# Kernel tuning notes

Hardware: AMD Instinct MI355X
Metric: run time of the kernel (lower is better)

The kernel has to match this reference:

```python
import jax, jax.numpy as jnp
import numpy as np

NUM_LAYERS = 16
ALPHA = 1.0
EPS = 1e-20

def setup_inputs() -> dict:
    key = jax.random.key(0)
    k1, k2, k3, k4 = jax.random.split(key, 4)
    B, S, M, G = 8, 9, 8, 512
    M2 = M * M
    return {
        "dict_real": jax.random.normal(k1, (B, S, M2, G), dtype=jnp.float32),
        "dict_imag": jax.random.normal(k2, (B, S, M2, G), dtype=jnp.float32),
        "cov_real": jax.random.normal(k3, (B, S, M, M), dtype=jnp.float32),
        "cov_imag": jax.random.normal(k4, (B, S, M, M), dtype=jnp.float32),
    }

def reference(dict_real, dict_imag, cov_real, cov_imag):
    D = (dict_real + 1j * dict_imag).astype(jnp.complex64)   # (B,S,M2,G) dictionary_band
    C = (cov_real + 1j * cov_imag).astype(jnp.complex64)     # (B,S,M,M) covariance matrix
    B, S, M, _ = C.shape
    G = D.shape[-1]
    # covariance_vector = cov.transpose(2,3).reshape(B,S,M2,1)
    r = jnp.swapaxes(C, 2, 3).reshape(B, S, M * M, 1)
    Dh = jnp.conj(jnp.swapaxes(D, 2, 3))                     # (B,S,G,M2)
    DhD = jnp.matmul(Dh, D)                                  # (B,S,G,G) Hermitian PSD
    Dhr = jnp.matmul(Dh, r)                                  # (B,S,G,1)
    # initial spectrum: real part, L2-normalized over grid dim
    res = jnp.real(Dhr).astype(jnp.float32)
    res = res / (jnp.linalg.norm(res, axis=2, keepdims=True) + EPS)
    # gamma = 1 / max|eig(D^H D)|; Hermitian PSD so eigvalsh gives same max magnitude
    eig = jnp.linalg.eigvalsh(DhD)                           # (B,S,G) real
    gamma = 1.0 / jnp.max(jnp.abs(eig), axis=2, keepdims=True)        # (B,S,1)
    lam = 0.5 * jnp.max(jnp.abs(Dhr), axis=2, keepdims=True).reshape(B, S, 1)
    theta = (ALPHA * lam * gamma).reshape(B, S, 1, 1)
    g = gamma.reshape(B, S, 1, 1).astype(jnp.complex64)
    I = jnp.eye(G, dtype=jnp.complex64)
    Wt = I - g * DhD                                         # (B,S,G,G)
    Wer = g * Dhr                                            # We @ r, constant per layer

    def step(res_c, _):
        s = jnp.matmul(Wt, res_c.astype(jnp.complex64)) + Wer
        res_new = jax.nn.relu(jnp.abs(s) - theta)            # soft-shrinkage on magnitude
        return res_new, res_new

    res_final, res_all = jax.lax.scan(step, res, None, length=NUM_LAYERS)
    result_init_all = jnp.moveaxis(res_all, 0, 2)            # (B,S,L,G,1)

    def minmax_norm(x):
        lo = jnp.min(x, axis=2, keepdims=True)
        hi = jnp.max(x, axis=2, keepdims=True)
        return (x - lo) / (hi - lo + EPS)

    result_ave = minmax_norm(jnp.mean(res_final, axis=1, keepdims=True).astype(jnp.float32))
    result = minmax_norm(res_final)
    return (result, result_ave, result_init_all)
```

## Files before the change

kernel.cpp:

```cpp
#include <hip/hip_runtime.h>
#include <math.h>

#define N_SQ   7
#define INV_P  (1.0f / 256.0f)
#define EPS_F  1e-20f
#define PH     72
#define PQ     67
#define PJ     1040

typedef _Float16 h2   __attribute__((ext_vector_type(2)));
typedef _Float16 f16x4 __attribute__((ext_vector_type(4)));
typedef _Float16 f16x8 __attribute__((ext_vector_type(8)));
typedef float    f32x4 __attribute__((ext_vector_type(4)));

__device__ inline float cdot2(h2 a, h2 b, float c) {
#if __has_builtin(__builtin_amdgcn_fdot2)
    return __builtin_amdgcn_fdot2(a, b, c, false);
#else
    return c + (float)a.x * (float)b.x + (float)a.y * (float)b.y;
#endif
}


__global__ __launch_bounds__(512, 1) void ista_main_kernel(
    const float* __restrict__ Dre, const float* __restrict__ Dim,
    const float* __restrict__ Cre, const float* __restrict__ Cim,
    float* __restrict__ out, float* __restrict__ ws)
{
    const int bs = blockIdx.x;
    const int t  = threadIdx.x;
    const int wv = t >> 6;
    const int ln = t & 63;
    const int c16 = ln & 15;
    const int qd  = ln >> 4;
    const float* __restrict__ dre = Dre + (size_t)bs * 32768;
    const float* __restrict__ dim = Dim + (size_t)bs * 32768;

    __shared__ __align__(16) float uBuf[9216];
    _Float16* ShRe = (_Float16*)uBuf;
    _Float16* ShIm = (_Float16*)uBuf + 64 * PH;
    float*    Q1   = uBuf + 4608;
    float*    sP   = uBuf;
    __shared__ __align__(16) float s_res[512];
    __shared__ __align__(16) float s_r[128];
    __shared__ float s_red[16];
    __shared__ float s_scal[8];

    if (t < 64) {
        int i = t >> 3, j = t & 7;
        s_r[2 * t]     = Cre[bs * 64 + j * 8 + i];
        s_r[2 * t + 1] = Cim[bs * 64 + j * 8 + i];
    }
    __syncthreads();

    float dhr_re = 0.f, dhr_im = 0.f;
    #pragma unroll 8
    for (int m = 0; m < 64; ++m) {
        float ar = dre[m * 512 + t], ai = dim[m * 512 + t];
        float rr = s_r[2 * m], ri = s_r[2 * m + 1];
        dhr_re += ar * rr + ai * ri;
        dhr_im += ar * ri - ai * rr;
    }
    {
        float sv = dhr_re * dhr_re;
        float mv = sqrtf(dhr_re * dhr_re + dhr_im * dhr_im);
        for (int off = 32; off; off >>= 1) {
            sv += __shfl_down(sv, off, 64);
            mv = fmaxf(mv, __shfl_down(mv, off, 64));
        }
        if (ln == 0) { s_red[wv] = sv; s_red[8 + wv] = mv; }
        __syncthreads();
        if (t == 0) {
            float ss = 0.f, mm = 0.f;
            for (int k = 0; k < 8; ++k) { ss += s_red[k]; mm = fmaxf(mm, s_red[8 + k]); }
            s_scal[7] = ss; s_scal[2] = mm;
        }
        __syncthreads();
    }
    float res_g = dhr_re / (sqrtf(s_scal[7]) + EPS_F);
    s_res[t] = res_g;

    const int tau0 = 2 * wv, tau1 = 2 * wv + 1;
    const int I0 = tau0 >> 2, J0 = tau0 & 3;
    const int I1 = tau1 >> 2, J1 = tau1 & 3;

    auto epilogue = [&](f32x4 P0, f32x4 Qa0, f32x4 P1, f32x4 Qa1, bool first, bool last) {
        #pragma unroll
        for (int r = 0; r < 4; ++r) {
            Q1[(I0 * 16 + qd * 4 + r) * PQ + J0 * 16 + c16] = Qa0[r];
            Q1[(I1 * 16 + qd * 4 + r) * PQ + J1 * 16 + c16] = Qa1[r];
        }
        float dv = 0.f;
        if (I0 == J0) {
            #pragma unroll
            for (int r = 0; r < 4; ++r) if (qd * 4 + r == c16) dv = fmaxf(dv, fabsf(P0[r]));
        }
        if (I1 == J1) {
            #pragma unroll
            for (int r = 0; r < 4; ++r) if (qd * 4 + r == c16) dv = fmaxf(dv, fabsf(P1[r]));
        }
        for (int off = 32; off; off >>= 1) dv = fmaxf(dv, __shfl_down(dv, off, 64));
        if (ln == 0) s_red[wv] = dv;
        __syncthreads();
        if (t == 0) {
            float m = 0.f;
            for (int k = 0; k < 8; ++k) m = fmaxf(m, s_red[k]);
            s_scal[3] = first ? logf(m) : 2.f * s_scal[3] + logf(m);
            s_scal[4] = 1.f / m;
        }
        __syncthreads();
        float ic = s_scal[4];
        float ci0[4], ci1[4];
        #pragma unroll
        for (int r = 0; r < 4; ++r) {
            ci0[r] = Qa0[r] - Q1[(J0 * 16 + c16) * PQ + I0 * 16 + qd * 4 + r];
            ci1[r] = Qa1[r] - Q1[(J1 * 16 + c16) * PQ + I1 * 16 + qd * 4 + r];
        }
        if (!last) {
            #pragma unroll
            for (int r = 0; r < 4; ++r) {
                ShRe[(I0 * 16 + qd * 4 + r) * PH + J0 * 16 + c16] = (_Float16)(P0[r] * ic);
                ShIm[(I0 * 16 + qd * 4 + r) * PH + J0 * 16 + c16] = (_Float16)(ci0[r] * ic);
                ShRe[(I1 * 16 + qd * 4 + r) * PH + J1 * 16 + c16] = (_Float16)(P1[r] * ic);
                ShIm[(I1 * 16 + qd * 4 + r) * PH + J1 * 16 + c16] = (_Float16)(ci1[r] * ic);
            }
            __syncthreads();
        } else {
            float fr = 0.f;
            #pragma unroll
            for (int r = 0; r < 4; ++r)
                fr += P0[r] * P0[r] + ci0[r] * ci0[r] + P1[r] * P1[r] + ci1[r] * ci1[r];
            fr *= ic * ic;
            for (int off = 32; off; off >>= 1) fr += __shfl_down(fr, off, 64);
            if (ln == 0) s_red[wv] = fr;
            __syncthreads();
            if (t == 0) {
                float fsum = 0.f;
                for (int k = 0; k < 8; ++k) fsum += s_red[k];
                float loglam = (2.f * s_scal[3] + logf(fsum)) * INV_P;
                float gamma = expf(-loglam);
                s_scal[0] = gamma;
                s_scal[1] = 0.5f * s_scal[2] * gamma;
            }
            __syncthreads();
        }
    };

    f32x4 gP0 = {0.f, 0.f, 0.f, 0.f}, gQ0 = {0.f, 0.f, 0.f, 0.f};
    f32x4 gP1 = {0.f, 0.f, 0.f, 0.f}, gQ1 = {0.f, 0.f, 0.f, 0.f};
    {
        const int srow = t >> 4;
        const int scb  = (t & 15) * 4;
        float4 pr0, pi0, pr1, pi1;
        pr0 = *(const float4*)&dre[srow * 512 + scb];
        pi0 = *(const float4*)&dim[srow * 512 + scb];
        pr1 = *(const float4*)&dre[(srow + 32) * 512 + scb];
        pi1 = *(const float4*)&dim[(srow + 32) * 512 + scb];
        for (int ch = 0; ch < 8; ++ch) {
            *(f16x4*)&ShRe[srow * PH + scb] =
                f16x4{(_Float16)pr0.x, (_Float16)pr0.y, (_Float16)pr0.z, (_Float16)pr0.w};
            *(f16x4*)&ShIm[srow * PH + scb] =
                f16x4{(_Float16)pi0.x, (_Float16)pi0.y, (_Float16)pi0.z, (_Float16)pi0.w};
            *(f16x4*)&ShRe[(srow + 32) * PH + scb] =
                f16x4{(_Float16)pr1.x, (_Float16)pr1.y, (_Float16)pr1.z, (_Float16)pr1.w};
            *(f16x4*)&ShIm[(srow + 32) * PH + scb] =
                f16x4{(_Float16)pi1.x, (_Float16)pi1.y, (_Float16)pi1.z, (_Float16)pi1.w};
            if (ch < 7) {
                int gc = (ch + 1) * 64;
                pr0 = *(const float4*)&dre[srow * 512 + gc + scb];
                pi0 = *(const float4*)&dim[srow * 512 + gc + scb];
                pr1 = *(const float4*)&dre[(srow + 32) * 512 + gc + scb];
                pi1 = *(const float4*)&dim[(srow + 32) * 512 + gc + scb];
            }
            __syncthreads();
            #pragma unroll
            for (int ks = 0; ks < 64; ks += 32) {
                f16x8 arI0 = *(const f16x8*)&ShRe[(I0 * 16 + c16) * PH + ks + qd * 8];
                f16x8 aiI0 = *(const f16x8*)&ShIm[(I0 * 16 + c16) * PH + ks + qd * 8];
                f16x8 arJ0 = *(const f16x8*)&ShRe[(J0 * 16 + c16) * PH + ks + qd * 8];
                f16x8 aiJ0 = *(const f16x8*)&ShIm[(J0 * 16 + c16) * PH + ks + qd * 8];
                gP0 = __builtin_amdgcn_mfma_f32_16x16x32_f16(arI0, arJ0, gP0, 0, 0, 0);
                gP0 = __builtin_amdgcn_mfma_f32_16x16x32_f16(aiI0, aiJ0, gP0, 0, 0, 0);
                gQ0 = __builtin_amdgcn_mfma_f32_16x16x32_f16(aiI0, arJ0, gQ0, 0, 0, 0);
                f16x8 arI1 = *(const f16x8*)&ShRe[(I1 * 16 + c16) * PH + ks + qd * 8];
                f16x8 aiI1 = *(const f16x8*)&ShIm[(I1 * 16 + c16) * PH + ks + qd * 8];
                f16x8 arJ1 = *(const f16x8*)&ShRe[(J1 * 16 + c16) * PH + ks + qd * 8];
                f16x8 aiJ1 = *(const f16x8*)&ShIm[(J1 * 16 + c16) * PH + ks + qd * 8];
                gP1 = __builtin_amdgcn_mfma_f32_16x16x32_f16(arI1, arJ1, gP1, 0, 0, 0);
                gP1 = __builtin_amdgcn_mfma_f32_16x16x32_f16(aiI1, aiJ1, gP1, 0, 0, 0);
                gQ1 = __builtin_amdgcn_mfma_f32_16x16x32_f16(aiI1, arJ1, gQ1, 0, 0, 0);
            }
            __syncthreads();
        }
    }
    epilogue(gP0, gQ0, gP1, gQ1, true, false);

    for (int sq = 0; sq < N_SQ; ++sq) {
        f32x4 P0 = {0.f, 0.f, 0.f, 0.f}, Qa0 = {0.f, 0.f, 0.f, 0.f};
        f32x4 P1 = {0.f, 0.f, 0.f, 0.f}, Qa1 = {0.f, 0.f, 0.f, 0.f};
        #pragma unroll
        for (int ks = 0; ks < 64; ks += 32) {
            f16x8 arI0 = *(const f16x8*)&ShRe[(I0 * 16 + c16) * PH + ks + qd * 8];
            f16x8 aiI0 = *(const f16x8*)&ShIm[(I0 * 16 + c16) * PH + ks + qd * 8];
            f16x8 arJ0 = *(const f16x8*)&ShRe[(J0 * 16 + c16) * PH + ks + qd * 8];
            f16x8 aiJ0 = *(const f16x8*)&ShIm[(J0 * 16 + c16) * PH + ks + qd * 8];
            P0  = __builtin_amdgcn_mfma_f32_16x16x32_f16(arI0, arJ0, P0, 0, 0, 0);
            P0  = __builtin_amdgcn_mfma_f32_16x16x32_f16(aiI0, aiJ0, P0, 0, 0, 0);
            Qa0 = __builtin_amdgcn_mfma_f32_16x16x32_f16(aiI0, arJ0, Qa0, 0, 0, 0);
            f16x8 arI1 = *(const f16x8*)&ShRe[(I1 * 16 + c16) * PH + ks + qd * 8];
            f16x8 aiI1 = *(const f16x8*)&ShIm[(I1 * 16 + c16) * PH + ks + qd * 8];
            f16x8 arJ1 = *(const f16x8*)&ShRe[(J1 * 16 + c16) * PH + ks + qd * 8];
            f16x8 aiJ1 = *(const f16x8*)&ShIm[(J1 * 16 + c16) * PH + ks + qd * 8];
            P1  = __builtin_amdgcn_mfma_f32_16x16x32_f16(arI1, arJ1, P1, 0, 0, 0);
            P1  = __builtin_amdgcn_mfma_f32_16x16x32_f16(aiI1, aiJ1, P1, 0, 0, 0);
            Qa1 = __builtin_amdgcn_mfma_f32_16x16x32_f16(aiI1, arJ1, Qa1, 0, 0, 0);
        }
        epilogue(P0, Qa0, P1, Qa1, false, sq == N_SQ - 1);
    }

    h2 dP[8][8];
    #pragma unroll
    for (int k = 0; k < 8; ++k) {
        const float4* pr = (const float4*)&dre[(8 * wv + k) * 512 + 8 * ln];
        const float4* pi = (const float4*)&dim[(8 * wv + k) * 512 + 8 * ln];
        float4 x0 = pr[0], x1 = pr[1], y0 = pi[0], y1 = pi[1];
        dP[k][0] = h2{(_Float16)x0.x, (_Float16)y0.x};
        dP[k][1] = h2{(_Float16)x0.y, (_Float16)y0.y};
        dP[k][2] = h2{(_Float16)x0.z, (_Float16)y0.z};
        dP[k][3] = h2{(_Float16)x0.w, (_Float16)y0.w};
        dP[k][4] = h2{(_Float16)x1.x, (_Float16)y1.x};
        dP[k][5] = h2{(_Float16)x1.y, (_Float16)y1.y};
        dP[k][6] = h2{(_Float16)x1.z, (_Float16)y1.z};
        dP[k][7] = h2{(_Float16)x1.w, (_Float16)y1.w};
    }

    const float gamma = s_scal[0];
    const float theta = s_scal[1];
    float* out_init = out + 40960 + (size_t)bs * 8192;
    const bool b5 = (ln & 32) != 0, b4 = (ln & 16) != 0, b3 = (ln & 8) != 0;

    for (int l = 0; l < 16; ++l) {
        float4 q0 = *(const float4*)&s_res[8 * ln];
        float4 q1 = *(const float4*)&s_res[8 * ln + 4];
        float rsv[8] = {q0.x, q0.y, q0.z, q0.w, q1.x, q1.y, q1.z, q1.w};
        float uR[8] = {0.f}, uI[8] = {0.f};
        #pragma unroll
        for (int j = 0; j < 8; ++j) {
            _Float16 rh = (_Float16)rsv[j];
            h2 hA = h2{rh, (_Float16)0.f};
            h2 hB = h2{(_Float16)0.f, rh};
            #pragma unroll
            for (int k = 0; k < 8; ++k) {
                uR[k] = cdot2(dP[k][j], hA, uR[k]);
                uI[k] = cdot2(dP[k][j], hB, uI[k]);
            }
        }
        float sR4[4], sI4[4];
        #pragma unroll
        for (int k = 0; k < 4; ++k) {
            float sendR = b5 ? uR[k] : uR[k + 4];
            float sendI = b5 ? uI[k] : uI[k + 4];
            float keepR = b5 ? uR[k + 4] : uR[k];
            float keepI = b5 ? uI[k + 4] : uI[k];
            sR4[k] = keepR + __shfl_xor(sendR, 32, 64);
            sI4[k] = keepI + __shfl_xor(sendI, 32, 64);
        }
        float tR2[2], tI2[2];
        #pragma unroll
        for (int k = 0; k < 2; ++k) {
            float sendR = b4 ? sR4[k] : sR4[k + 2];
            float sendI = b4 ? sI4[k] : sI4[k + 2];
            float keepR = b4 ? sR4[k + 2] : sR4[k];
            float keepI = b4 ? sI4[k + 2] : sI4[k];
            tR2[k] = keepR + __shfl_xor(sendR, 16, 64);
            tI2[k] = keepI + __shfl_xor(sendI, 16, 64);
        }
        float fR = (b3 ? tR2[1] : tR2[0]) + __shfl_xor(b3 ? tR2[0] : tR2[1], 8, 64);
        float fI = (b3 ? tI2[1] : tI2[0]) + __shfl_xor(b3 ? tI2[0] : tI2[1], 8, 64);
        fR += __shfl_xor(fR, 4, 64); fI += __shfl_xor(fI, 4, 64);
        fR += __shfl_xor(fR, 2, 64); fI += __shfl_xor(fI, 2, 64);
        fR += __shfl_xor(fR, 1, 64); fI += __shfl_xor(fI, 1, 64);
        h2 hu1[8], hu2[8];
        #pragma unroll
        for (int m = 0; m < 8; ++m) {
            float br = __shfl(fR, 8 * m, 64);
            float bi = __shfl(fI, 8 * m, 64);
            hu1[m] = h2{(_Float16)br, (_Float16)bi};
            hu2[m] = h2{(_Float16)bi, (_Float16)(-br)};
        }
        #pragma unroll
        for (int j = 0; j < 8; ++j) {
            float wr = 0.f, wi = 0.f;
            #pragma unroll
            for (int k = 0; k < 8; ++k) {
                wr = cdot2(dP[k][j], hu1[k], wr);
                wi = cdot2(dP[k][j], hu2[k], wi);
            }
            *(float2*)&sP[j * PJ + wv * 130 + 2 * ln] = make_float2(wr, wi);
        }
        __syncthreads();
        float wR = 0.f, wI = 0.f;
        {
            const float* pp = &sP[(t & 7) * PJ + 2 * (t >> 3)];
            #pragma unroll
            for (int w8 = 0; w8 < 8; ++w8) {
                float2 c = *(const float2*)(pp + w8 * 130);
                wR += c.x; wI += c.y;
            }
        }
        float sre = res_g + gamma * (dhr_re - wR);
        float sim = gamma * (dhr_im - wI);
        float mag = sqrtf(sre * sre + sim * sim);
        res_g = fmaxf(mag - theta, 0.f);
        out_init[l * 512 + t] = res_g;
        s_res[t] = res_g;
        __syncthreads();
    }

    {
        float mn = res_g, mx = res_g;
        for (int off = 32; off; off >>= 1) {
            mn = fminf(mn, __shfl_down(mn, off, 64));
            mx = fmaxf(mx, __shfl_down(mx, off, 64));
        }
        if (ln == 0) { s_red[wv] = mn; s_red[8 + wv] = mx; }
        __syncthreads();
        if (t == 0) {
            float a = s_red[0], b2 = s_red[8];
            for (int k = 1; k < 8; ++k) { a = fminf(a, s_red[k]); b2 = fmaxf(b2, s_red[8 + k]); }
            s_scal[5] = a; s_scal[6] = b2;
        }
        __syncthreads();
        out[bs * 512 + t] = (res_g - s_scal[5]) / (s_scal[6] - s_scal[5] + EPS_F);
        ws[bs * 512 + t] = res_g;
    }
}

__global__ __launch_bounds__(512) void ista_ave_kernel(
    const float* __restrict__ ws, float* __restrict__ out)
{
    const int b = blockIdx.x;
    const int g = threadIdx.x;
    __shared__ float s_red[16];
    __shared__ float s_scal[2];
    float acc = 0.f;
    #pragma unroll
    for (int s = 0; s < 9; ++s) acc += ws[(b * 9 + s) * 512 + g];
    acc *= (1.f / 9.f);
    float mn = acc, mx = acc;
    for (int off = 32; off; off >>= 1) {
        mn = fminf(mn, __shfl_down(mn, off, 64));
        mx = fmaxf(mx, __shfl_down(mx, off, 64));
    }
    if ((g & 63) == 0) { s_red[g >> 6] = mn; s_red[8 + (g >> 6)] = mx; }
    __syncthreads();
    if (g == 0) {
        float a = s_red[0], b2 = s_red[8];
        for (int k = 1; k < 8; ++k) { a = fminf(a, s_red[k]); b2 = fmaxf(b2, s_red[8 + k]); }
        s_scal[0] = a; s_scal[1] = b2;
    }
    __syncthreads();
    out[36864 + b * 512 + g] = (acc - s_scal[0]) / (s_scal[1] - s_scal[0] + EPS_F);
}

extern "C" void kernel_launch(void* const* d_in, const int* in_sizes, int n_in,
                              void* d_out, int out_size, void* d_ws, size_t ws_size,
                              hipStream_t stream) {
    const float* Dre = (const float*)d_in[0];
    const float* Dim = (const float*)d_in[1];
    const float* Cre = (const float*)d_in[2];
    const float* Cim = (const float*)d_in[3];
    float* out = (float*)d_out;
    float* ws  = (float*)d_ws;

    ista_main_kernel<<<72, 512, 0, stream>>>(Dre, Dim, Cre, Cim, out, ws);
    ista_ave_kernel<<<8, 512, 0, stream>>>(ws, out);
}
```

Measured before the change: 134.2 us.

## Restructure ISTA matvec with register-resident dictionary slices and LDS reductions

The per-layer product D^H(D r) is reorganised. Each thread now keeps its grid column of D as packed fp16 pairs in registers, and each wave keeps a 64-grid chunk of D captured from the staged shared-memory tiles. The D·r partials are reduced across waves through LDS by wave 0, then every thread computes its own output with fdot2. This replaces the old shuffle-based butterfly reduction, the global reloads of D, and the cross-wave LDS transpose. It costs about 128 more VGPRs of resident dictionary data and adds a serialised wave-0 reduction step between two barriers.

```diff
diff --git a/kernel.cpp b/kernel.cpp
--- a/kernel.cpp
+++ b/kernel.cpp
@@ -6,10 +6,8 @@
 #define EPS_F  1e-20f
 #define PH     72
 #define PQ     67
-#define PJ     1040
-
-typedef _Float16 h2   __attribute__((ext_vector_type(2)));
-typedef _Float16 f16x4 __attribute__((ext_vector_type(4)));
+
+typedef _Float16 h2    __attribute__((ext_vector_type(2)));
 typedef _Float16 f16x8 __attribute__((ext_vector_type(8)));
 typedef float    f32x4 __attribute__((ext_vector_type(4)));
 
@@ -20,6 +18,9 @@
     return c + (float)a.x * (float)b.x + (float)a.y * (float)b.y;
 #endif
 }
+__device__ inline h2 bch2(unsigned int x) { return __builtin_bit_cast(h2, x); }
+__device__ inline h2 bch2f(float x)       { return __builtin_bit_cast(h2, x); }
+__device__ inline float bcf(h2 x)         { return __builtin_bit_cast(float, x); }
 
 
 __global__ __launch_bounds__(512, 1) void ista_main_kernel(
@@ -40,8 +41,9 @@
     _Float16* ShRe = (_Float16*)uBuf;
     _Float16* ShIm = (_Float16*)uBuf + 64 * PH;
     float*    Q1   = uBuf + 4608;
-    float*    sP   = uBuf;
-    __shared__ __align__(16) float s_res[512];
+    float*    sUp  = uBuf;
+    float*    sHu  = uBuf + 1024;
+    _Float16* sResH = (_Float16*)(uBuf + 1152);
     __shared__ __align__(16) float s_r[128];
     __shared__ float s_red[16];
     __shared__ float s_scal[8];
@@ -54,9 +56,11 @@
     __syncthreads();
 
     float dhr_re = 0.f, dhr_im = 0.f;
-    #pragma unroll 8
+    h2 dV[64];
+    #pragma unroll
     for (int m = 0; m < 64; ++m) {
         float ar = dre[m * 512 + t], ai = dim[m * 512 + t];
+        dV[m] = h2{(_Float16)ar, (_Float16)ai};
         float rr = s_r[2 * m], ri = s_r[2 * m + 1];
         dhr_re += ar * rr + ai * ri;
         dhr_im += ar * ri - ai * rr;
@@ -78,7 +82,6 @@
         __syncthreads();
     }
     float res_g = dhr_re / (sqrtf(s_scal[7]) + EPS_F);
-    s_res[t] = res_g;
 
     const int tau0 = 2 * wv, tau1 = 2 * wv + 1;
     const int I0 = tau0 >> 2, J0 = tau0 & 3;
@@ -146,6 +149,7 @@
         }
     };
 
+    h2 du_re[32], du_im[32];
     f32x4 gP0 = {0.f, 0.f, 0.f, 0.f}, gQ0 = {0.f, 0.f, 0.f, 0.f};
     f32x4 gP1 = {0.f, 0.f, 0.f, 0.f}, gQ1 = {0.f, 0.f, 0.f, 0.f};
     {
@@ -157,14 +161,14 @@
         pr1 = *(const float4*)&dre[(srow + 32) * 512 + scb];
         pi1 = *(const float4*)&dim[(srow + 32) * 512 + scb];
         for (int ch = 0; ch < 8; ++ch) {
-            *(f16x4*)&ShRe[srow * PH + scb] =
-                f16x4{(_Float16)pr0.x, (_Float16)pr0.y, (_Float16)pr0.z, (_Float16)pr0.w};
-            *(f16x4*)&ShIm[srow * PH + scb] =
-                f16x4{(_Float16)pi0.x, (_Float16)pi0.y, (_Float16)pi0.z, (_Float16)pi0.w};
-            *(f16x4*)&ShRe[(srow + 32) * PH + scb] =
-                f16x4{(_Float16)pr1.x, (_Float16)pr1.y, (_Float16)pr1.z, (_Float16)pr1.w};
-            *(f16x4*)&ShIm[(srow + 32) * PH + scb] =
-                f16x4{(_Float16)pi1.x, (_Float16)pi1.y, (_Float16)pi1.z, (_Float16)pi1.w};
+            *(h2*)&ShRe[srow * PH + scb]     = h2{(_Float16)pr0.x, (_Float16)pr0.y};
+            *(h2*)&ShRe[srow * PH + scb + 2] = h2{(_Float16)pr0.z, (_Float16)pr0.w};
+            *(h2*)&ShIm[srow * PH + scb]     = h2{(_Float16)pi0.x, (_Float16)pi0.y};
+            *(h2*)&ShIm[srow * PH + scb + 2] = h2{(_Float16)pi0.z, (_Float16)pi0.w};
+            *(h2*)&ShRe[(srow + 32) * PH + scb]     = h2{(_Float16)pr1.x, (_Float16)pr1.y};
+            *(h2*)&ShRe[(srow + 32) * PH + scb + 2] = h2{(_Float16)pr1.z, (_Float16)pr1.w};
+            *(h2*)&ShIm[(srow + 32) * PH + scb]     = h2{(_Float16)pi1.x, (_Float16)pi1.y};
+            *(h2*)&ShIm[(srow + 32) * PH + scb + 2] = h2{(_Float16)pi1.z, (_Float16)pi1.w};
             if (ch < 7) {
                 int gc = (ch + 1) * 64;
                 pr0 = *(const float4*)&dre[srow * 512 + gc + scb];
@@ -190,6 +194,17 @@
                 gP1 = __builtin_amdgcn_mfma_f32_16x16x32_f16(aiI1, aiJ1, gP1, 0, 0, 0);
                 gQ1 = __builtin_amdgcn_mfma_f32_16x16x32_f16(aiI1, arJ1, gQ1, 0, 0, 0);
             }
+            if (ch == wv) {
+                #pragma unroll
+                for (int c = 0; c < 8; ++c) {
+                    uint4 aw = *(const uint4*)&ShRe[ln * PH + 8 * c];
+                    du_re[4 * c + 0] = bch2(aw.x); du_re[4 * c + 1] = bch2(aw.y);
+                    du_re[4 * c + 2] = bch2(aw.z); du_re[4 * c + 3] = bch2(aw.w);
+                    uint4 bw = *(const uint4*)&ShIm[ln * PH + 8 * c];
+                    du_im[4 * c + 0] = bch2(bw.x); du_im[4 * c + 1] = bch2(bw.y);
+                    du_im[4 * c + 2] = bch2(bw.z); du_im[4 * c + 3] = bch2(bw.w);
+                }
+            }
             __syncthreads();
         }
     }
@@ -218,103 +233,51 @@
         epilogue(P0, Qa0, P1, Qa1, false, sq == N_SQ - 1);
     }
 
-    h2 dP[8][8];
-    #pragma unroll
-    for (int k = 0; k < 8; ++k) {
-        const float4* pr = (const float4*)&dre[(8 * wv + k) * 512 + 8 * ln];
-        const float4* pi = (const float4*)&dim[(8 * wv + k) * 512 + 8 * ln];
-        float4 x0 = pr[0], x1 = pr[1], y0 = pi[0], y1 = pi[1];
-        dP[k][0] = h2{(_Float16)x0.x, (_Float16)y0.x};
-        dP[k][1] = h2{(_Float16)x0.y, (_Float16)y0.y};
-        dP[k][2] = h2{(_Float16)x0.z, (_Float16)y0.z};
-        dP[k][3] = h2{(_Float16)x0.w, (_Float16)y0.w};
-        dP[k][4] = h2{(_Float16)x1.x, (_Float16)y1.x};
-        dP[k][5] = h2{(_Float16)x1.y, (_Float16)y1.y};
-        dP[k][6] = h2{(_Float16)x1.z, (_Float16)y1.z};
-        dP[k][7] = h2{(_Float16)x1.w, (_Float16)y1.w};
-    }
-
     const float gamma = s_scal[0];
     const float theta = s_scal[1];
     float* out_init = out + 40960 + (size_t)bs * 8192;
-    const bool b5 = (ln & 32) != 0, b4 = (ln & 16) != 0, b3 = (ln & 8) != 0;
+    const int resh_base = 64 * wv;
 
     for (int l = 0; l < 16; ++l) {
-        float4 q0 = *(const float4*)&s_res[8 * ln];
-        float4 q1 = *(const float4*)&s_res[8 * ln + 4];
-        float rsv[8] = {q0.x, q0.y, q0.z, q0.w, q1.x, q1.y, q1.z, q1.w};
-        float uR[8] = {0.f}, uI[8] = {0.f};
-        #pragma unroll
-        for (int j = 0; j < 8; ++j) {
-            _Float16 rh = (_Float16)rsv[j];
-            h2 hA = h2{rh, (_Float16)0.f};
-            h2 hB = h2{(_Float16)0.f, rh};
-            #pragma unroll
-            for (int k = 0; k < 8; ++k) {
-                uR[k] = cdot2(dP[k][j], hA, uR[k]);
-                uI[k] = cdot2(dP[k][j], hB, uI[k]);
-            }
-        }
-        float sR4[4], sI4[4];
-        #pragma unroll
-        for (int k = 0; k < 4; ++k) {
-            float sendR = b5 ? uR[k] : uR[k + 4];
-            float sendI = b5 ? uI[k] : uI[k + 4];
-            float keepR = b5 ? uR[k + 4] : uR[k];
-            float keepI = b5 ? uI[k + 4] : uI[k];
-            sR4[k] = keepR + __shfl_xor(sendR, 32, 64);
-            sI4[k] = keepI + __shfl_xor(sendI, 32, 64);
-        }
-        float tR2[2], tI2[2];
-        #pragma unroll
-        for (int k = 0; k < 2; ++k) {
-            float sendR = b4 ? sR4[k] : sR4[k + 2];
-            float sendI = b4 ? sI4[k] : sI4[k + 2];
-            float keepR = b4 ? sR4[k + 2] : sR4[k];
-            float keepI = b4 ? sI4[k + 2] : sI4[k];
-            tR2[k] = keepR + __shfl_xor(sendR, 16, 64);
-            tI2[k] = keepI + __shfl_xor(sendI, 16, 64);
-        }
-        float fR = (b3 ? tR2[1] : tR2[0]) + __shfl_xor(b3 ? tR2[0] : tR2[1], 8, 64);
-        float fI = (b3 ? tI2[1] : tI2[0]) + __shfl_xor(b3 ? tI2[0] : tI2[1], 8, 64);
-        fR += __shfl_xor(fR, 4, 64); fI += __shfl_xor(fI, 4, 64);
-        fR += __shfl_xor(fR, 2, 64); fI += __shfl_xor(fI, 2, 64);
-        fR += __shfl_xor(fR, 1, 64); fI += __shfl_xor(fI, 1, 64);
-        h2 hu1[8], hu2[8];
-        #pragma unroll
-        for (int m = 0; m < 8; ++m) {
-            float br = __shfl(fR, 8 * m, 64);
-            float bi = __shfl(fI, 8 * m, 64);
-            hu1[m] = h2{(_Float16)br, (_Float16)bi};
-            hu2[m] = h2{(_Float16)bi, (_Float16)(-br)};
-        }
-        #pragma unroll
-        for (int j = 0; j < 8; ++j) {
-            float wr = 0.f, wi = 0.f;
-            #pragma unroll
-            for (int k = 0; k < 8; ++k) {
-                wr = cdot2(dP[k][j], hu1[k], wr);
-                wi = cdot2(dP[k][j], hu2[k], wi);
-            }
-            *(float2*)&sP[j * PJ + wv * 130 + 2 * ln] = make_float2(wr, wi);
+        sResH[t] = (_Float16)res_g;
+        float upR = 0.f, upI = 0.f;
+        #pragma unroll
+        for (int c = 0; c < 8; ++c) {
+            uint4 rw = *(const uint4*)&sResH[resh_base + 8 * c];
+            h2 r0 = bch2(rw.x), r1 = bch2(rw.y), r2 = bch2(rw.z), r3 = bch2(rw.w);
+            upR = cdot2(du_re[4 * c + 0], r0, upR);  upI = cdot2(du_im[4 * c + 0], r0, upI);
+            upR = cdot2(du_re[4 * c + 1], r1, upR);  upI = cdot2(du_im[4 * c + 1], r1, upI);
+            upR = cdot2(du_re[4 * c + 2], r2, upR);  upI = cdot2(du_im[4 * c + 2], r2, upI);
+            upR = cdot2(du_re[4 * c + 3], r3, upR);  upI = cdot2(du_im[4 * c + 3], r3, upI);
+        }
+        *(float2*)&sUp[(wv * 64 + ln) * 2] = make_float2(upR, upI);
+        __syncthreads();
+        if (wv == 0) {
+            float ufR = 0.f, ufI = 0.f;
+            #pragma unroll
+            for (int w8 = 0; w8 < 8; ++w8) {
+                float2 p = *(const float2*)&sUp[(w8 * 64 + ln) * 2];
+                ufR += p.x; ufI += p.y;
+            }
+            h2 hu1 = h2{(_Float16)ufR, (_Float16)ufI};
+            h2 hu2 = h2{(_Float16)ufI, (_Float16)(-ufR)};
+            *(float2*)&sHu[2 * ln] = make_float2(bcf(hu1), bcf(hu2));
         }
         __syncthreads();
         float wR = 0.f, wI = 0.f;
-        {
-            const float* pp = &sP[(t & 7) * PJ + 2 * (t >> 3)];
-            #pragma unroll
-            for (int w8 = 0; w8 < 8; ++w8) {
-                float2 c = *(const float2*)(pp + w8 * 130);
-                wR += c.x; wI += c.y;
-            }
+        #pragma unroll
+        for (int mm = 0; mm < 32; ++mm) {
+            float4 hq = *(const float4*)&sHu[4 * mm];
+            wR = cdot2(dV[2 * mm],     bch2f(hq.x), wR);
+            wI = cdot2(dV[2 * mm],     bch2f(hq.y), wI);
+            wR = cdot2(dV[2 * mm + 1], bch2f(hq.z), wR);
+            wI = cdot2(dV[2 * mm + 1], bch2f(hq.w), wI);
         }
         float sre = res_g + gamma * (dhr_re - wR);
         float sim = gamma * (dhr_im - wI);
         float mag = sqrtf(sre * sre + sim * sim);
         res_g = fmaxf(mag - theta, 0.f);
         out_init[l * 512 + t] = res_g;
-        s_res[t] = res_g;
-        __syncthreads();
     }
 
     {
```

Result: faster. 112.6 us (-16.1%).
